# Optimization experiments

Hardware: AMD Instinct MI355X
Metric: run time of the kernel (lower is better)

Reference implementation:

```python
import jax
import jax.numpy as jnp
import numpy as np
from jax import lax

DIM = 48
HIDDEN = int(DIM * 2.66)  # 127, matches torch int(dim*ffn_expansion_factor)
EPS_LN = 1e-5
EPS_NORM = 1e-12


def conv2d(x, w, groups=1):
    # x: NCHW, w: OIHW, stride 1, SAME padding (all kernels here are 1x1 or 3x3 pad=1)
    return lax.conv_general_dilated(
        x, w, window_strides=(1, 1), padding='SAME',
        feature_group_count=groups,
        dimension_numbers=('NCHW', 'OIHW', 'NCHW'))


def layernorm_cbias(x, w, b):
    # Restormer WithBias_LayerNorm: normalize over channel dim (biased var)
    mu = jnp.mean(x, axis=1, keepdims=True)
    var = jnp.mean(jnp.square(x - mu), axis=1, keepdims=True)
    xn = (x - mu) * lax.rsqrt(var + EPS_LN)
    return xn * w[None, :, None, None] + b[None, :, None, None]


def l2norm_last(x):
    # torch F.normalize(dim=-1, eps=1e-12)
    n = jnp.sqrt(jnp.sum(jnp.square(x), axis=-1, keepdims=True))
    return x / jnp.maximum(n, EPS_NORM)


def setup_inputs() -> dict:
    key = jax.random.key(0)
    ks = jax.random.split(key, 16)
    s = 0.05
    B, H, W = 2, 512, 512
    return {
        'x': jax.random.normal(ks[0], (B, 3, H, W), dtype=jnp.float32),
        # OverlapPatchEmbed: Conv2d(3, 48, 3, pad=1, bias=False)
        'pe_w': jax.random.normal(ks[1], (DIM, 3, 3, 3), dtype=jnp.float32) * s,
        # norm1 (WithBias)
        'n1_w': jnp.ones((DIM,), dtype=jnp.float32),
        'n1_b': jnp.zeros((DIM,), dtype=jnp.float32),
        # MDTA attention, num_heads=1
        'temp': jnp.ones((1, 1, 1), dtype=jnp.float32),
        'qkv_w': jax.random.normal(ks[2], (DIM * 3, DIM, 1, 1), dtype=jnp.float32) * s,
        'qkv_dw_w': jax.random.normal(ks[3], (DIM * 3, 1, 3, 3), dtype=jnp.float32) * s,
        'po_w': jax.random.normal(ks[4], (DIM, DIM, 1, 1), dtype=jnp.float32) * s,
        # norm2
        'n2_w': jnp.ones((DIM,), dtype=jnp.float32),
        'n2_b': jnp.zeros((DIM,), dtype=jnp.float32),
        # GDFN
        'pi_w': jax.random.normal(ks[5], (HIDDEN * 2, DIM, 1, 1), dtype=jnp.float32) * s,
        'ffn_dw_w': jax.random.normal(ks[6], (HIDDEN * 2, 1, 3, 3), dtype=jnp.float32) * s,
        'fo_w': jax.random.normal(ks[7], (DIM, HIDDEN, 1, 1), dtype=jnp.float32) * s,
    }


def reference(x, pe_w, n1_w, n1_b, temp, qkv_w, qkv_dw_w, po_w, n2_w, n2_b, pi_w, ffn_dw_w, fo_w):
    # Patch embed
    patch = conv2d(x, pe_w)  # [B, 48, H, W]
    B, C, H, W = patch.shape

    # ---- MDTA channel attention on norm1(patch) ----
    y = layernorm_cbias(patch, n1_w, n1_b)
    qkv = conv2d(conv2d(y, qkv_w), qkv_dw_w, groups=3 * C)  # [B, 3C, H, W]
    q, k, v = jnp.split(qkv, 3, axis=1)
    # heads=1: rearrange to [B, C, H*W]
    q = l2norm_last(q.reshape(B, C, H * W))
    k = l2norm_last(k.reshape(B, C, H * W))
    v = v.reshape(B, C, H * W)
    attn = jax.nn.softmax(jnp.einsum('bcn,bdn->bcd', q, k) * temp[0, 0, 0], axis=-1)  # [B, C, C]
    out = jnp.einsum('bcd,bdn->bcn', attn, v).reshape(B, C, H, W)
    attn_out = conv2d(out, po_w)
    first = patch + attn_out

    # ---- GDFN on norm2(first) ----
    y2 = layernorm_cbias(first, n2_w, n2_b)
    h = conv2d(conv2d(y2, pi_w), ffn_dw_w, groups=2 * HIDDEN)  # [B, 254, H, W]
    x1, x2 = jnp.split(h, 2, axis=1)
    ffn = conv2d(jax.nn.gelu(x1, approximate=False) * x2, fo_w)
    return first + ffn  # second_residual [B, 48, H, W]
```

## Files before the change

kernel.cpp:

```cpp
#include <hip/hip_runtime.h>
#include <hip/hip_bf16.h>
#include <math.h>

#define HW 512
#define NPIX (HW*HW)

typedef __hip_bfloat16 bf16;
typedef __attribute__((ext_vector_type(8))) unsigned short u16x8;
typedef __attribute__((ext_vector_type(8))) short s16x8;
typedef __attribute__((ext_vector_type(4))) float f32x4;

__device__ __forceinline__ float b2f(bf16 v) { return __bfloat162float(v); }
__device__ __forceinline__ bf16 f2b(float v) { return __float2bfloat16(v); }

union fu { float f; unsigned int u; };
union bu { bf16 b; unsigned short u; };

__device__ __forceinline__ void ld_bf8(const bf16* p, float* f) {
    u16x8 u = *(const u16x8*)p;
#pragma unroll
    for (int j = 0; j < 8; j++) { fu c; c.u = ((unsigned int)u[j]) << 16; f[j] = c.f; }
}

__device__ __forceinline__ void st_bf8(bf16* p, const float* f) {
    u16x8 u;
#pragma unroll
    for (int j = 0; j < 8; j++) { bu c; c.b = f2b(f[j]); u[j] = c.u; }
    *(u16x8*)p = u;
}

__global__ __launch_bounds__(256) void k_prep(const float* __restrict__ qkvw,
                                              const float* __restrict__ piw,
                                              const float* __restrict__ fow,
                                              bf16* __restrict__ WQ,
                                              bf16* __restrict__ WP,
                                              bf16* __restrict__ WF,
                                              float* __restrict__ Z0,
                                              float* __restrict__ Z1)
{
    int idx = blockIdx.x*256 + threadIdx.x;
    if (idx < 9216) {
        int oc = idx >> 6, k = idx & 63;
        WQ[idx] = f2b(k < 48 ? qkvw[oc*48 + k] : 0.f);
    } else if (idx < 25600) {
        int j = idx - 9216; int oc = j >> 6, k = j & 63;
        WP[j] = f2b((oc < 254 && k < 48) ? piw[oc*48 + k] : 0.f);
    } else if (idx < 31744) {
        int j = idx - 25600; int oc = j >> 7, k = j & 127;
        WF[j] = f2b(k < 127 ? fow[oc*127 + k] : 0.f);
    } else if (idx < 36544) {
        int j = idx - 31744;
        if (j < 2400) Z0[j] = 0.f; else Z1[j-2400] = 0.f;
    }
}

__global__ __launch_bounds__(256) void k_pe(const float* __restrict__ x,
                                            const float* __restrict__ w,
                                            bf16* __restrict__ out)
{
    __shared__ float ws[48*27];
    for (int i = threadIdx.x; i < 48*27; i += 256) ws[i] = w[i];
    __syncthreads();
    int lane = threadIdx.x & 63, wv = threadIdx.x >> 6;
    int row = blockIdx.x*4 + wv;
    int col = lane*8;
    float a[3][3][8];
    float lf[3][3], rt[3][3];
#pragma unroll
    for (int c = 0; c < 3; c++)
#pragma unroll
        for (int r = 0; r < 3; r++) {
            int rr = row + r - 1;
            if (rr >= 0 && rr < HW) {
                const float* p = x + (size_t)c*NPIX + rr*HW + col;
                float4 u0 = *(const float4*)p, u1 = *(const float4*)(p+4);
                a[c][r][0]=u0.x; a[c][r][1]=u0.y; a[c][r][2]=u0.z; a[c][r][3]=u0.w;
                a[c][r][4]=u1.x; a[c][r][5]=u1.y; a[c][r][6]=u1.z; a[c][r][7]=u1.w;
            } else {
#pragma unroll
                for (int j = 0; j < 8; j++) a[c][r][j] = 0.f;
            }
            float l = __shfl_up(a[c][r][7], 1);  lf[c][r] = (lane==0)  ? 0.f : l;
            float rv= __shfl_down(a[c][r][0],1); rt[c][r] = (lane==63) ? 0.f : rv;
        }
    for (int oc = 0; oc < 48; oc++) {
        float acc[8];
#pragma unroll
        for (int j = 0; j < 8; j++) acc[j] = 0.f;
#pragma unroll
        for (int c = 0; c < 3; c++)
#pragma unroll
            for (int r = 0; r < 3; r++) {
                float w0 = ws[oc*27 + c*9 + r*3 + 0];
                float w1 = ws[oc*27 + c*9 + r*3 + 1];
                float w2 = ws[oc*27 + c*9 + r*3 + 2];
#pragma unroll
                for (int j = 0; j < 8; j++) {
                    float xm = (j==0) ? lf[c][r] : a[c][r][j-1];
                    float x0 = a[c][r][j];
                    float xp = (j==7) ? rt[c][r] : a[c][r][j+1];
                    acc[j] += w0*xm + w1*x0 + w2*xp;
                }
            }
        st_bf8(out + (size_t)oc*NPIX + row*HW + col, acc);
    }
}

template<int OC_PAD, int OC_REAL, int MT_PER_WAVE>
__global__ __launch_bounds__(256) void k_ln_mm_mfma(const bf16* __restrict__ in,
                                                    const float* __restrict__ lnw,
                                                    const float* __restrict__ lnb,
                                                    const s16x8* __restrict__ wpad,
                                                    bf16* __restrict__ out)
{
    constexpr int NMT = OC_PAD/16;
    __shared__ s16x8 y_lds[256*8];
    __shared__ unsigned short stage[OC_PAD][72];
    int t = threadIdx.x;
    int base = blockIdx.x*256;
    int px = base + t;
    float y[48];
    float mu = 0.f;
#pragma unroll
    for (int i = 0; i < 48; i++) { y[i] = b2f(in[(size_t)i*NPIX + px]); mu += y[i]; }
    mu *= (1.f/48.f);
    float var = 0.f;
#pragma unroll
    for (int i = 0; i < 48; i++) { float d = y[i]-mu; var += d*d; }
    float s = rsqrtf(var*(1.f/48.f) + 1e-5f);
#pragma unroll
    for (int i = 0; i < 48; i++) y[i] = (y[i]-mu)*s*lnw[i] + lnb[i];
#pragma unroll
    for (int kb = 0; kb < 8; kb++) {
        union { s16x8 v; unsigned short us[8]; } pk;
#pragma unroll
        for (int j = 0; j < 8; j++) {
            int c = kb*8 + j;
            bu b; b.b = f2b(c < 48 ? y[c] : 0.f);
            pk.us[j] = (c < 48) ? b.u : (unsigned short)0;
        }
        y_lds[t*8 + (kb ^ (t & 7))] = pk.v;
    }
    __syncthreads();

    int lane = t & 63, wv = t >> 6;
    int q = lane >> 4, n = lane & 15;
    s16x8 a[MT_PER_WAVE][2];
#pragma unroll
    for (int mi = 0; mi < MT_PER_WAVE; mi++) {
        int mt = wv + 4*mi;
        if (mt < NMT) {
            int oc = mt*16 + n;
            a[mi][0] = wpad[oc*8 + q];
            a[mi][1] = wpad[oc*8 + 4 + q];
        }
    }
#pragma unroll 1
    for (int g = 0; g < 4; g++) {
#pragma unroll
        for (int sub = 0; sub < 4; sub++) {
            int nt = g*4 + sub;
            int npx = nt*16 + n;
            s16x8 b0 = y_lds[npx*8 + (q ^ (npx & 7))];
            s16x8 b1 = y_lds[npx*8 + ((4 + q) ^ (npx & 7))];
#pragma unroll
            for (int mi = 0; mi < MT_PER_WAVE; mi++) {
                int mt = wv + 4*mi;
                if (mt >= NMT) continue;
                f32x4 acc = {0.f, 0.f, 0.f, 0.f};
                acc = __builtin_amdgcn_mfma_f32_16x16x32_bf16(a[mi][0], b0, acc, 0, 0, 0);
                acc = __builtin_amdgcn_mfma_f32_16x16x32_bf16(a[mi][1], b1, acc, 0, 0, 0);
                int ocb = mt*16 + q*4;
#pragma unroll
                for (int r = 0; r < 4; r++) {
                    bu bb; bb.b = f2b(acc[r]);
                    stage[ocb + r][sub*16 + n] = bb.u;
                }
            }
        }
        __syncthreads();
        if (t < OC_REAL) {
            const u16x8* sp = (const u16x8*)stage[t];
            u16x8 c0 = sp[0], c1 = sp[1], c2 = sp[2], c3 = sp[3];
            u16x8 c4 = sp[4], c5 = sp[5], c6 = sp[6], c7 = sp[7];
            u16x8* op = (u16x8*)(out + (size_t)t*NPIX + base + g*64);
            op[0] = c0; op[1] = c1; op[2] = c2; op[3] = c3;
            op[4] = c4; op[5] = c5; op[6] = c6; op[7] = c7;
        }
        __syncthreads();
    }
}

__global__ __launch_bounds__(256) void k_dw(const bf16* __restrict__ in,
                                            const float* __restrict__ w,
                                            bf16* __restrict__ out)
{
    int ch = blockIdx.y;
    int lane = threadIdx.x & 63, wv = threadIdx.x >> 6;
    int row0 = blockIdx.x*32 + wv*8;
    int col = lane*8;
    const bf16* ip = in + (size_t)ch*NPIX;
    bf16* op = out + (size_t)ch*NPIX;
    float wk[9];
#pragma unroll
    for (int i = 0; i < 9; i++) wk[i] = w[ch*9+i];
    float a[3][8];
    float lf[3], rt[3];

    auto loadrow = [&](int s, int rr) {
        if (rr >= 0 && rr < HW) ld_bf8(ip + rr*HW + col, a[s]);
        else {
#pragma unroll
            for (int j = 0; j < 8; j++) a[s][j] = 0.f;
        }
        float l = __shfl_up(a[s][7], 1);  lf[s] = (lane==0)  ? 0.f : l;
        float rv= __shfl_down(a[s][0],1); rt[s] = (lane==63) ? 0.f : rv;
    };
    loadrow(0, row0-1);
    loadrow(1, row0);
#pragma unroll
    for (int r = 0; r < 8; r++) {
        loadrow((r+2)%3, row0 + r + 1);
        const int s0 = r%3, s1 = (r+1)%3, s2 = (r+2)%3;
        float o[8];
#pragma unroll
        for (int j = 0; j < 8; j++) {
            float sm = 0.f;
#pragma unroll
            for (int kr = 0; kr < 3; kr++) {
                const int ss = (kr==0) ? s0 : (kr==1) ? s1 : s2;
                float xm = (j==0) ? lf[ss] : a[ss][j-1];
                float x0 = a[ss][j];
                float xp = (j==7) ? rt[ss] : a[ss][j+1];
                sm += wk[kr*3+0]*xm + wk[kr*3+1]*x0 + wk[kr*3+2]*xp;
            }
            o[j] = sm;
        }
        st_bf8(op + (row0 + r)*HW + col, o);
    }
}

__global__ __launch_bounds__(512) void k_qkt(const bf16* __restrict__ qm,
                                             const bf16* __restrict__ km,
                                             float* __restrict__ S,
                                             float* __restrict__ sumsq)
{
    __shared__ float Sp[8][48][52];
    __shared__ float ssp[8][96];
    int t = threadIdx.x;
    int lane = t & 63, wv = t >> 6;
    int qg = lane >> 4, n = lane & 15;
    size_t px0 = (size_t)(blockIdx.x*8 + wv) * 128 + qg*8;

    f32x4 acc[3][3];
#pragma unroll
    for (int i = 0; i < 3; i++)
#pragma unroll
        for (int j = 0; j < 3; j++) acc[i][j] = (f32x4){0.f, 0.f, 0.f, 0.f};
    float sq[3] = {0.f, 0.f, 0.f}, sk[3] = {0.f, 0.f, 0.f};

#pragma unroll 2
    for (int s = 0; s < 4; s++) {
        size_t p = px0 + s*32;
        s16x8 qa[3], ka[3];
#pragma unroll
        for (int i = 0; i < 3; i++) {
            qa[i] = *(const s16x8*)&qm[(size_t)(16*i + n)*NPIX + p];
            ka[i] = *(const s16x8*)&km[(size_t)(16*i + n)*NPIX + p];
        }
#pragma unroll
        for (int i = 0; i < 3; i++)
#pragma unroll
            for (int j = 0; j < 3; j++)
                acc[i][j] = __builtin_amdgcn_mfma_f32_16x16x32_bf16(qa[i], ka[j], acc[i][j], 0, 0, 0);
#pragma unroll
        for (int i = 0; i < 3; i++) {
            union { s16x8 v; unsigned short us[8]; } uq, uk;
            uq.v = qa[i]; uk.v = ka[i];
#pragma unroll
            for (int j = 0; j < 8; j++) {
                fu cq; cq.u = ((unsigned int)uq.us[j]) << 16; sq[i] += cq.f*cq.f;
                fu ck; ck.u = ((unsigned int)uk.us[j]) << 16; sk[i] += ck.f*ck.f;
            }
        }
    }

#pragma unroll
    for (int i = 0; i < 3; i++)
#pragma unroll
        for (int j = 0; j < 3; j++)
#pragma unroll
            for (int r = 0; r < 4; r++)
                Sp[wv][16*i + qg*4 + r][16*j + n] = acc[i][j][r];
#pragma unroll
    for (int i = 0; i < 3; i++) {
        float a = sq[i], b = sk[i];
        a += __shfl_down(a, 32); a += __shfl_down(a, 16);
        b += __shfl_down(b, 32); b += __shfl_down(b, 16);
        if (lane < 16) { ssp[wv][16*i + lane] = a; ssp[wv][48 + 16*i + lane] = b; }
    }
    __syncthreads();

    for (int idx = t; idx < 2304; idx += 512) {
        int r = idx / 48, c = idx - r*48;
        float v = 0.f;
#pragma unroll
        for (int w = 0; w < 8; w++) v += Sp[w][r][c];
        atomicAdd(&S[idx], v);
    }
    if (t < 96) {
        float v = 0.f;
#pragma unroll
        for (int w = 0; w < 8; w++) v += ssp[w][t];
        atomicAdd(&sumsq[t], v);
    }
}

__global__ __launch_bounds__(256) void k_attn_final(const float* __restrict__ S,
                                                    const float* __restrict__ sumsq,
                                                    const float* __restrict__ po_w,
                                                    const float* __restrict__ temp,
                                                    float* __restrict__ M)
{
    __shared__ float attn[48][48];
    __shared__ float nrm[96];
    int t = threadIdx.x;
    if (t < 96) nrm[t] = fmaxf(sqrtf(sumsq[t]), 1e-12f);
    __syncthreads();
    float tmp = temp[0];
    if (t < 48) {
        float row[48];
        float mx = -1e30f;
#pragma unroll
        for (int d = 0; d < 48; d++) {
            float l = S[t*48+d] / (nrm[t]*nrm[48+d]) * tmp;
            row[d] = l; mx = fmaxf(mx, l);
        }
        float sum = 0.f;
#pragma unroll
        for (int d = 0; d < 48; d++) { float e = expf(row[d]-mx); sum += e; row[d] = e; }
        float inv = 1.f/sum;
#pragma unroll
        for (int d = 0; d < 48; d++) attn[t][d] = row[d]*inv;
    }
    __syncthreads();
    for (int idx = t; idx < 2304; idx += 256) {
        int cp = idx/48, d = idx%48;
        float acc = 0.f;
#pragma unroll
        for (int c = 0; c < 48; c++) acc += po_w[cp*48+c] * attn[c][d];
        M[idx] = acc;
    }
}

__global__ __launch_bounds__(256) void k_attnv(const bf16* __restrict__ v,
                                               const float* __restrict__ M,
                                               bf16* __restrict__ patch)
{
    __shared__ float Ms[48*48];
    for (int i = threadIdx.x; i < 2304; i += 256) Ms[i] = M[i];
    __syncthreads();
    int p = (blockIdx.x*256 + threadIdx.x)*2;
    float v0[48], v1[48];
#pragma unroll
    for (int i = 0; i < 48; i++) {
        unsigned int word = *(const unsigned int*)&v[(size_t)i*NPIX + p];
        fu c0, c1; c0.u = word << 16; c1.u = word & 0xffff0000u;
        v0[i] = c0.f; v1[i] = c1.f;
    }
    for (int oc = 0; oc < 48; oc++) {
        const float4* wr = (const float4*)&Ms[oc*48];
        float a0 = 0.f, a1 = 0.f;
#pragma unroll
        for (int i = 0; i < 12; i++) {
            float4 w4 = wr[i];
            a0 += w4.x*v0[4*i] + w4.y*v0[4*i+1] + w4.z*v0[4*i+2] + w4.w*v0[4*i+3];
            a1 += w4.x*v1[4*i] + w4.y*v1[4*i+1] + w4.z*v1[4*i+2] + w4.w*v1[4*i+3];
        }
        unsigned int* pp = (unsigned int*)&patch[(size_t)oc*NPIX + p];
        unsigned int old = *pp;
        fu f0, f1; f0.u = old << 16; f1.u = old & 0xffff0000u;
        bu b0, b1; b0.b = f2b(f0.f + a0); b1.b = f2b(f1.f + a1);
        *pp = (unsigned int)b0.u | ((unsigned int)b1.u << 16);
    }
}

__global__ __launch_bounds__(256) void k_dw_glu(const bf16* __restrict__ h1,
                                                const float* __restrict__ w,
                                                bf16* __restrict__ g)
{
    int ch = blockIdx.y;
    int lane = threadIdx.x & 63, wv = threadIdx.x >> 6;
    int row0 = blockIdx.x*32 + wv*8;
    int col = lane*8;
    float w1[9], w2[9];
#pragma unroll
    for (int i = 0; i < 9; i++) { w1[i] = w[ch*9+i]; w2[i] = w[(ch+127)*9+i]; }
    const bf16* i1 = h1 + (size_t)ch*NPIX;
    const bf16* i2 = h1 + (size_t)(ch+127)*NPIX;
    bf16* op = g + (size_t)ch*NPIX;
    float aa[3][8], bb[3][8];
    float lfa[3], rta[3], lfb[3], rtb[3];

    auto loadrow = [&](int s, int rr) {
        if (rr >= 0 && rr < HW) {
            ld_bf8(i1 + rr*HW + col, aa[s]);
            ld_bf8(i2 + rr*HW + col, bb[s]);
        } else {
#pragma unroll
            for (int j = 0; j < 8; j++) { aa[s][j] = 0.f; bb[s][j] = 0.f; }
        }
        float l1 = __shfl_up(aa[s][7],1);   lfa[s] = (lane==0)  ? 0.f : l1;
        float r1 = __shfl_down(aa[s][0],1); rta[s] = (lane==63) ? 0.f : r1;
        float l2 = __shfl_up(bb[s][7],1);   lfb[s] = (lane==0)  ? 0.f : l2;
        float r2 = __shfl_down(bb[s][0],1); rtb[s] = (lane==63) ? 0.f : r2;
    };
    loadrow(0, row0-1);
    loadrow(1, row0);
#pragma unroll
    for (int r = 0; r < 8; r++) {
        loadrow((r+2)%3, row0 + r + 1);
        const int s0 = r%3, s1 = (r+1)%3, s2 = (r+2)%3;
        float o[8];
#pragma unroll
        for (int j = 0; j < 8; j++) {
            float sum1 = 0.f, sum2 = 0.f;
#pragma unroll
            for (int kr = 0; kr < 3; kr++) {
                const int ss = (kr==0) ? s0 : (kr==1) ? s1 : s2;
                float xm = (j==0) ? lfa[ss] : aa[ss][j-1];
                float x0 = aa[ss][j];
                float xp = (j==7) ? rta[ss] : aa[ss][j+1];
                sum1 += w1[kr*3+0]*xm + w1[kr*3+1]*x0 + w1[kr*3+2]*xp;
                float ym = (j==0) ? lfb[ss] : bb[ss][j-1];
                float y0 = bb[ss][j];
                float yp = (j==7) ? rtb[ss] : bb[ss][j+1];
                sum2 += w2[kr*3+0]*ym + w2[kr*3+1]*y0 + w2[kr*3+2]*yp;
            }
            float ge = 0.5f*sum1*(1.f + erff(sum1*0.70710678118654752f));
            o[j] = ge*sum2;
        }
        st_bf8(op + (row0 + r)*HW + col, o);
    }
}

__global__ __launch_bounds__(256) void k_fo_mfma(const bf16* __restrict__ g,
                                                 const s16x8* __restrict__ wfo,
                                                 const bf16* __restrict__ first,
                                                 float* __restrict__ out)
{
    __shared__ s16x8 glds[256*16];
    int t = threadIdx.x;
    int base = blockIdx.x*256;
    int px = base + t;
#pragma unroll
    for (int kb = 0; kb < 16; kb++) {
        union { s16x8 v; unsigned short us[8]; } pk;
#pragma unroll
        for (int j = 0; j < 8; j++) {
            int c = kb*8 + j;
            if (c < 127) { bu b; b.b = g[(size_t)c*NPIX + px]; pk.us[j] = b.u; }
            else pk.us[j] = 0;
        }
        glds[t*16 + (kb ^ (t & 15))] = pk.v;
    }
    __syncthreads();
    int lane = t & 63, wv = t >> 6;
    int q = lane >> 4, n = lane & 15;
    s16x8 a[3][4];
#pragma unroll
    for (int mt = 0; mt < 3; mt++) {
        int oc = mt*16 + n;
#pragma unroll
        for (int kc = 0; kc < 4; kc++)
            a[mt][kc] = wfo[oc*16 + kc*4 + q];
    }
#pragma unroll 1
    for (int ni = 0; ni < 4; ni++) {
        int nt = wv*4 + ni;
        int npx = nt*16 + n;
        s16x8 b[4];
#pragma unroll
        for (int kc = 0; kc < 4; kc++)
            b[kc] = glds[npx*16 + ((kc*4 + q) ^ (npx & 15))];
        size_t pxg = base + npx;
#pragma unroll
        for (int mt = 0; mt < 3; mt++) {
            f32x4 acc = {0.f, 0.f, 0.f, 0.f};
#pragma unroll
            for (int kc = 0; kc < 4; kc++)
                acc = __builtin_amdgcn_mfma_f32_16x16x32_bf16(a[mt][kc], b[kc], acc, 0, 0, 0);
            int ocb = mt*16 + q*4;
#pragma unroll
            for (int r = 0; r < 4; r++) {
                int oc = ocb + r;
                out[(size_t)oc*NPIX + pxg] = b2f(first[(size_t)oc*NPIX + pxg]) + acc[r];
            }
        }
    }
}

extern "C" void kernel_launch(void* const* d_in, const int* in_sizes, int n_in,
                              void* d_out, int out_size, void* d_ws, size_t ws_size,
                              hipStream_t stream)
{
    const float* x     = (const float*)d_in[0];
    const float* pe_w  = (const float*)d_in[1];
    const float* n1w   = (const float*)d_in[2];
    const float* n1b   = (const float*)d_in[3];
    const float* temp  = (const float*)d_in[4];
    const float* qkvw  = (const float*)d_in[5];
    const float* qkvdw = (const float*)d_in[6];
    const float* pow_  = (const float*)d_in[7];
    const float* n2w   = (const float*)d_in[8];
    const float* n2b   = (const float*)d_in[9];
    const float* piw   = (const float*)d_in[10];
    const float* ffndw = (const float*)d_in[11];
    const float* fow   = (const float*)d_in[12];
    float* out = (float*)d_out;

    bf16*  Pb = (bf16*)d_ws;
    bf16*  A  = Pb + (size_t)48*NPIX;
    bf16*  Bq = A + (size_t)144*NPIX;
    bf16*  H1 = A;
    bf16*  G  = A + (size_t)254*NPIX;
    bf16*  WQ = A + (size_t)381*NPIX;
    bf16*  WP = WQ + 144*64;
    bf16*  WF = WP + 256*64;
    float* SM0 = (float*)(A + (size_t)384*NPIX);
    float* SM1 = SM0 + 4704;

    dim3 blk(256);
    int nb1 = NPIX/256;
    int nb2 = NPIX/512;
    int nr  = HW/4;
    int nrw = HW/32;

    k_prep<<<dim3(143), blk, 0, stream>>>(qkvw, piw, fow, WQ, WP, WF, SM0, SM1);

    for (int b = 0; b < 2; b++) {
        const float* xb   = x   + (size_t)b*3*NPIX;
        float*       outb = out + (size_t)b*48*NPIX;
        float* SMb   = b ? SM1 : SM0;
        float* sumsq = SMb;
        float* S     = SMb + 96;
        float* M     = SMb + 2400;

        k_pe<<<dim3(nr), blk, 0, stream>>>(xb, pe_w, Pb);
        k_ln_mm_mfma<144,144,3><<<dim3(nb1), blk, 0, stream>>>(Pb, n1w, n1b, (const s16x8*)WQ, A);
        k_dw<<<dim3(nrw, 144), blk, 0, stream>>>(A, qkvdw, Bq);
        k_qkt<<<dim3(NPIX/1024), dim3(512), 0, stream>>>(Bq, Bq + (size_t)48*NPIX, S, sumsq);
        k_attn_final<<<dim3(1), blk, 0, stream>>>(S, sumsq, pow_, temp, M);
        k_attnv<<<dim3(nb2), blk, 0, stream>>>(Bq + (size_t)96*NPIX, M, Pb);
        k_ln_mm_mfma<256,254,4><<<dim3(nb1), blk, 0, stream>>>(Pb, n2w, n2b, (const s16x8*)WP, H1);
        k_dw_glu<<<dim3(nrw, 127), blk, 0, stream>>>(H1, ffndw, G);
        k_fo_mfma<<<dim3(nb1), blk, 0, stream>>>(G, (const s16x8*)WF, Pb, outb);
    }
}
```

Baseline: 727.2 us.

## Fuse norm1, qkv 1x1 conv and depthwise 3x3 into one tiled kernel

Replaces the separate LN+qkv-matmul kernel and depthwise conv kernel with a single kernel working on 8x32 pixel tiles with halo. LayerNorm output and the 144-channel pointwise result are kept in LDS, and the depthwise conv reads from LDS. This removes the write and re-read of the 144-channel intermediate tensor A in global memory. In exchange, the halo pixels (340 vs 256) are normalised and multiplied redundantly, and the large LDS footprint may limit occupancy.

```diff
diff --git a/kernel.cpp b/kernel.cpp
--- a/kernel.cpp
+++ b/kernel.cpp
@@ -15,6 +15,10 @@
 
 union fu { float f; unsigned int u; };
 union bu { bf16 b; unsigned short u; };
+
+__device__ __forceinline__ float us2f(unsigned short u) {
+    fu c; c.u = ((unsigned int)u) << 16; return c.f;
+}
 
 __device__ __forceinline__ void ld_bf8(const bf16* p, float* f) {
     u16x8 u = *(const u16x8*)p;
@@ -106,6 +110,119 @@
     }
 }
 
+#define YPAD 56
+#define APAD 360
+__global__ __launch_bounds__(256) void k_ln_dw(const bf16* __restrict__ patch,
+                                               const float* __restrict__ lnw,
+                                               const float* __restrict__ lnb,
+                                               const s16x8* __restrict__ wq,
+                                               const float* __restrict__ dww,
+                                               bf16* __restrict__ outq)
+{
+    __shared__ unsigned short y_lds[352*YPAD];
+    __shared__ unsigned short a_lds[48*APAD];
+    int t = threadIdx.x;
+    int c0 = blockIdx.x*32, r0 = blockIdx.y*8;
+
+    for (int hp = t; hp < 352; hp += 256) {
+        int hr = hp/34, hc = hp - hr*34;
+        int gr = r0 - 1 + hr, gc = c0 - 1 + hc;
+        bool ok = (hp < 340) && (gr >= 0) && (gr < HW) && (gc >= 0) && (gc < HW);
+        if (ok) {
+            int gpx = gr*HW + gc;
+            float y[48];
+            float mu = 0.f;
+#pragma unroll
+            for (int i = 0; i < 48; i++) { y[i] = b2f(patch[(size_t)i*NPIX + gpx]); mu += y[i]; }
+            mu *= (1.f/48.f);
+            float var = 0.f;
+#pragma unroll
+            for (int i = 0; i < 48; i++) { float d = y[i]-mu; var += d*d; }
+            float s = rsqrtf(var*(1.f/48.f) + 1e-5f);
+#pragma unroll
+            for (int i = 0; i < 48; i++) y[i] = (y[i]-mu)*s*lnw[i] + lnb[i];
+#pragma unroll
+            for (int kb = 0; kb < 6; kb++) {
+                union { u16x8 v; unsigned short us[8]; } pk;
+#pragma unroll
+                for (int j = 0; j < 8; j++) { bu b; b.b = f2b(y[kb*8+j]); pk.us[j] = b.u; }
+                *(u16x8*)&y_lds[hp*YPAD + kb*8] = pk.v;
+            }
+        } else {
+            u16x8 z = {0,0,0,0,0,0,0,0};
+#pragma unroll
+            for (int kb = 0; kb < 6; kb++) *(u16x8*)&y_lds[hp*YPAD + kb*8] = z;
+        }
+    }
+    __syncthreads();
+
+    int lane = t & 63, wv = t >> 6;
+    int q = lane >> 4, n = lane & 15;
+    int lr = lane >> 3, lc = lane & 7;
+
+#pragma unroll 1
+    for (int cc = 0; cc < 3; cc++) {
+        s16x8 a0[3], a1[3];
+#pragma unroll
+        for (int mi = 0; mi < 3; mi++) {
+            int oc = (cc*3 + mi)*16 + n;
+            a0[mi] = wq[oc*8 + q];
+            a1[mi] = wq[oc*8 + 4 + q];
+        }
+#pragma unroll 1
+        for (int nt = wv; nt < 22; nt += 4) {
+            int hp = nt*16 + n;
+            s16x8 b0 = *(const s16x8*)&y_lds[hp*YPAD + q*8];
+            s16x8 b1 = {0,0,0,0,0,0,0,0};
+            if (q < 2) b1 = *(const s16x8*)&y_lds[hp*YPAD + 32 + q*8];
+#pragma unroll
+            for (int mi = 0; mi < 3; mi++) {
+                f32x4 acc = {0.f, 0.f, 0.f, 0.f};
+                acc = __builtin_amdgcn_mfma_f32_16x16x32_bf16(a0[mi], b0, acc, 0, 0, 0);
+                acc = __builtin_amdgcn_mfma_f32_16x16x32_bf16(a1[mi], b1, acc, 0, 0, 0);
+                int mchb = mi*16 + q*4;
+#pragma unroll
+                for (int r = 0; r < 4; r++) {
+                    bu bb; bb.b = f2b(acc[r]);
+                    a_lds[(mchb + r)*APAD + hp] = bb.u;
+                }
+            }
+        }
+        __syncthreads();
+
+#pragma unroll 1
+        for (int i = 0; i < 12; i++) {
+            int mch = wv + 4*i;
+            int ch = cc*48 + mch;
+            float wk[9];
+#pragma unroll
+            for (int k = 0; k < 9; k++) wk[k] = dww[ch*9 + k];
+            const unsigned short* ap = &a_lds[mch*APAD];
+            float o[4];
+#pragma unroll
+            for (int j = 0; j < 4; j++) {
+                float sm = 0.f;
+#pragma unroll
+                for (int kr = 0; kr < 3; kr++) {
+                    int hb = (lr + kr)*34 + lc*4 + j;
+                    float xm = us2f(ap[hb]);
+                    float x0 = us2f(ap[hb + 1]);
+                    float xp = us2f(ap[hb + 2]);
+                    sm += wk[kr*3+0]*xm + wk[kr*3+1]*x0 + wk[kr*3+2]*xp;
+                }
+                o[j] = sm;
+            }
+            ushort4 pk;
+            { bu b; b.b = f2b(o[0]); pk.x = b.u; }
+            { bu b; b.b = f2b(o[1]); pk.y = b.u; }
+            { bu b; b.b = f2b(o[2]); pk.z = b.u; }
+            { bu b; b.b = f2b(o[3]); pk.w = b.u; }
+            *(ushort4*)&outq[(size_t)ch*NPIX + (r0 + lr)*HW + c0 + lc*4] = pk;
+        }
+        __syncthreads();
+    }
+}
+
 template<int OC_PAD, int OC_REAL, int MT_PER_WAVE>
 __global__ __launch_bounds__(256) void k_ln_mm_mfma(const bf16* __restrict__ in,
                                                     const float* __restrict__ lnw,
@@ -188,55 +305,6 @@
             op[4] = c4; op[5] = c5; op[6] = c6; op[7] = c7;
         }
         __syncthreads();
-    }
-}
-
-__global__ __launch_bounds__(256) void k_dw(const bf16* __restrict__ in,
-                                            const float* __restrict__ w,
-                                            bf16* __restrict__ out)
-{
-    int ch = blockIdx.y;
-    int lane = threadIdx.x & 63, wv = threadIdx.x >> 6;
-    int row0 = blockIdx.x*32 + wv*8;
-    int col = lane*8;
-    const bf16* ip = in + (size_t)ch*NPIX;
-    bf16* op = out + (size_t)ch*NPIX;
-    float wk[9];
-#pragma unroll
-    for (int i = 0; i < 9; i++) wk[i] = w[ch*9+i];
-    float a[3][8];
-    float lf[3], rt[3];
-
-    auto loadrow = [&](int s, int rr) {
-        if (rr >= 0 && rr < HW) ld_bf8(ip + rr*HW + col, a[s]);
-        else {
-#pragma unroll
-            for (int j = 0; j < 8; j++) a[s][j] = 0.f;
-        }
-        float l = __shfl_up(a[s][7], 1);  lf[s] = (lane==0)  ? 0.f : l;
-        float rv= __shfl_down(a[s][0],1); rt[s] = (lane==63) ? 0.f : rv;
-    };
-    loadrow(0, row0-1);
-    loadrow(1, row0);
-#pragma unroll
-    for (int r = 0; r < 8; r++) {
-        loadrow((r+2)%3, row0 + r + 1);
-        const int s0 = r%3, s1 = (r+1)%3, s2 = (r+2)%3;
-        float o[8];
-#pragma unroll
-        for (int j = 0; j < 8; j++) {
-            float sm = 0.f;
-#pragma unroll
-            for (int kr = 0; kr < 3; kr++) {
-                const int ss = (kr==0) ? s0 : (kr==1) ? s1 : s2;
-                float xm = (j==0) ? lf[ss] : a[ss][j-1];
-                float x0 = a[ss][j];
-                float xp = (j==7) ? rt[ss] : a[ss][j+1];
-                sm += wk[kr*3+0]*xm + wk[kr*3+1]*x0 + wk[kr*3+2]*xp;
-            }
-            o[j] = sm;
-        }
-        st_bf8(op + (row0 + r)*HW + col, o);
     }
 }
 
@@ -547,8 +615,7 @@
         float* M     = SMb + 2400;
 
         k_pe<<<dim3(nr), blk, 0, stream>>>(xb, pe_w, Pb);
-        k_ln_mm_mfma<144,144,3><<<dim3(nb1), blk, 0, stream>>>(Pb, n1w, n1b, (const s16x8*)WQ, A);
-        k_dw<<<dim3(nrw, 144), blk, 0, stream>>>(A, qkvdw, Bq);
+        k_ln_dw<<<dim3(HW/32, HW/8), blk, 0, stream>>>(Pb, n1w, n1b, (const s16x8*)WQ, qkvdw, Bq);
         k_qkt<<<dim3(NPIX/1024), dim3(512), 0, stream>>>(Bq, Bq + (size_t)48*NPIX, S, sumsq);
         k_attn_final<<<dim3(1), blk, 0, stream>>>(S, sumsq, pow_, temp, M);
         k_attnv<<<dim3(nb2), blk, 0, stream>>>(Bq + (size_t)96*NPIX, M, Pb);
```

After: 752.1 us. 1.03x slower.
